# Optimization experiments

Hardware: AMD Instinct MI355X
Metric: run time of the kernel (lower is better)

## Reference

```python
import jax, jax.numpy as jnp
import numpy as np

B, C = 8388608, 4
OTHERS_IDX = 3

def setup_inputs() -> dict:
    key = jax.random.key(0)
    k1, k2 = jax.random.split(key)
    preds = jax.random.normal(k1, (B, C), dtype=jnp.float32)
    target = jax.random.randint(k2, (B,), 0, C, dtype=jnp.int64)
    return {"preds": preds, "target": target, "others_idx": OTHERS_IDX}

def reference(preds, target, others_idx):
    # softmax over class dim (dim=1 in the torch module)
    probs = jax.nn.softmax(preds, axis=1)              # [B, C]
    p_o = probs[:, others_idx]                          # [B]
    s = probs.sum(axis=1)                               # [B] (== 1, but computed as in original)
    # per-sample false-negative error (samples whose target IS the 'others' class)
    fne_i = 0.5 * ((s - p_o) ** 2 + (p_o - 1.0) ** 2)   # [B]
    # per-sample false-positive error (samples whose target is NOT 'others')
    fpe_i = 0.5 * ((-p_o) ** 2 + p_o ** 2)              # [B]
    is_others = (target == others_idx)                  # [B] bool
    fne_num = jnp.sum(is_others).astype(probs.dtype)
    fpe_num = jnp.sum(~is_others).astype(probs.dtype)
    fne = jnp.sum(jnp.where(is_others, fne_i, 0.0)) / fne_num
    fpe = jnp.sum(jnp.where(is_others, 0.0, fpe_i)) / fpe_num
    return fpe + fne
```

## Files before the change

kernel.cpp:

```cpp
#include <hip/hip_runtime.h>


#define BLOCK 1024
#define ROWS 16
#define CHUNK 4
#define STAGES (ROWS / CHUNK)

typedef float vfloat4 __attribute__((ext_vector_type(4)));

__device__ __forceinline__ void mfe_row(vfloat4 x, int t, int o,
                                        float& fne_acc, float& fpe_acc,
                                        float& cnt_acc) {
    float m = fmaxf(fmaxf(x.x, x.y), fmaxf(x.z, x.w));
    float e0 = __expf(x.x - m);
    float e1 = __expf(x.y - m);
    float e2 = __expf(x.z - m);
    float e3 = __expf(x.w - m);
    float S = (e0 + e1) + (e2 + e3);
    float r = 1.0f / S;
    float p0 = e0 * r, p1 = e1 * r, p2 = e2 * r, p3 = e3 * r;
    float s = ((p0 + p1) + p2) + p3;
    float po = (o == 0) ? p0 : (o == 1) ? p1 : (o == 2) ? p2 : p3;

    float d1 = s - po;
    float d2 = po - 1.0f;
    float fne_i = 0.5f * (d1 * d1 + d2 * d2);
    float fpe_i = po * po;

    bool is_o = (t == o);
    fne_acc += is_o ? fne_i : 0.0f;
    fpe_acc += is_o ? 0.0f : fpe_i;
    cnt_acc += is_o ? 1.0f : 0.0f;
}

__global__ __launch_bounds__(BLOCK) void mfe_partial(
    const vfloat4* __restrict__ preds,
    const int* __restrict__ target,
    const int* __restrict__ others_idx_p,
    float* __restrict__ fne_part,
    float* __restrict__ fpe_part,
    float* __restrict__ cnt_part,
    int n_rows)
{
    const int o = *others_idx_p;
    int tid = blockIdx.x * BLOCK + threadIdx.x;
    int nth = gridDim.x * BLOCK;

    float fne_acc = 0.0f, fpe_acc = 0.0f, cnt_acc = 0.0f;

    if (tid + (ROWS - 1) * nth < n_rows) {
        vfloat4 xbuf[2][CHUNK];
        int     tbuf[2][CHUNK];

        #pragma unroll
        for (int k = 0; k < CHUNK; ++k) {
            int i = tid + k * nth;
            xbuf[0][k] = __builtin_nontemporal_load(&preds[i]);
            tbuf[0][k] = __builtin_nontemporal_load(&target[i]);
        }

        #pragma unroll
        for (int s = 0; s < STAGES; ++s) {
            int cur = s & 1;
            int nxt = cur ^ 1;
            if (s + 1 < STAGES) {
                #pragma unroll
                for (int k = 0; k < CHUNK; ++k) {
                    int i = tid + ((s + 1) * CHUNK + k) * nth;
                    xbuf[nxt][k] = __builtin_nontemporal_load(&preds[i]);
                    tbuf[nxt][k] = __builtin_nontemporal_load(&target[i]);
                }
            }
            __builtin_amdgcn_sched_barrier(0);
            #pragma unroll
            for (int k = 0; k < CHUNK; ++k)
                mfe_row(xbuf[cur][k], tbuf[cur][k], o, fne_acc, fpe_acc, cnt_acc);
        }
    } else {
        for (int i = tid; i < n_rows; i += nth)
            mfe_row(preds[i], target[i], o, fne_acc, fpe_acc, cnt_acc);
    }

    #pragma unroll
    for (int off = 32; off > 0; off >>= 1) {
        fne_acc += __shfl_down(fne_acc, off, 64);
        fpe_acc += __shfl_down(fpe_acc, off, 64);
        cnt_acc += __shfl_down(cnt_acc, off, 64);
    }

    if ((threadIdx.x & 63) == 0) {
        int part = blockIdx.x * (BLOCK / 64) + (threadIdx.x >> 6);
        fne_part[part] = fne_acc;
        fpe_part[part] = fpe_acc;
        cnt_part[part] = cnt_acc;
    }
}

__global__ __launch_bounds__(1024) void mfe_final(
    const float* __restrict__ fne_part,
    const float* __restrict__ fpe_part,
    const float* __restrict__ cnt_part,
    int nparts, int n_rows, float* __restrict__ out)
{
    double fn = 0.0, fp = 0.0, c = 0.0;
    for (int i = threadIdx.x; i < nparts; i += blockDim.x) {
        fn += (double)fne_part[i];
        fp += (double)fpe_part[i];
        c  += (double)cnt_part[i];
    }
    #pragma unroll
    for (int off = 32; off > 0; off >>= 1) {
        fn += __shfl_down(fn, off, 64);
        fp += __shfl_down(fp, off, 64);
        c  += __shfl_down(c, off, 64);
    }
    __shared__ double s_fn[16], s_fp[16], s_c[16];
    int wave = threadIdx.x >> 6;
    int lane = threadIdx.x & 63;
    if (lane == 0) { s_fn[wave] = fn; s_fp[wave] = fp; s_c[wave] = c; }
    __syncthreads();

    if (threadIdx.x == 0) {
        double tfn = 0.0, tfp = 0.0, tc = 0.0;
        int nwaves = blockDim.x >> 6;
        for (int w = 0; w < nwaves; ++w) { tfn += s_fn[w]; tfp += s_fp[w]; tc += s_c[w]; }
        double fne_num = tc;
        double fpe_num = (double)n_rows - fne_num;
        double res = 0.0;
        if (fpe_num > 0.0) res += tfp / fpe_num;
        if (fne_num > 0.0) res += tfn / fne_num;
        out[0] = (float)res;
    }
}

extern "C" void kernel_launch(void* const* d_in, const int* in_sizes, int n_in,
                              void* d_out, int out_size, void* d_ws, size_t ws_size,
                              hipStream_t stream) {
    const vfloat4* preds = (const vfloat4*)d_in[0];
    const int* target = (const int*)d_in[1];
    const int* others_idx = (const int*)d_in[2];
    float* out = (float*)d_out;

    int n_rows = in_sizes[0] / 4;

    int grid = (n_rows + BLOCK * ROWS - 1) / (BLOCK * ROWS);
    int nparts = grid * (BLOCK / 64);

    float* fne_part = (float*)d_ws;
    float* fpe_part = fne_part + nparts;
    float* cnt_part = fpe_part + nparts;

    mfe_partial<<<grid, BLOCK, 0, stream>>>(preds, target, others_idx,
                                            fne_part, fpe_part, cnt_part, n_rows);
    mfe_final<<<1, 1024, 0, stream>>>(fne_part, fpe_part, cnt_part,
                                      nparts, n_rows, out);
}
```

Before: 202.9 us.

## Fuse final reduction into main kernel via last-block atomic ticket

Replaces the two-kernel reduction with a single kernel. Each block reduces its per-wave partials in shared memory, writes one double per quantity, and takes an atomic ticket. The last block to arrive performs the final reduction and writes the output. This removes the second kernel launch and its gap, but adds a memset launch for the ticket plus a fence and an atomic per block.

```diff
diff --git a/kernel.cpp b/kernel.cpp
--- a/kernel.cpp
+++ b/kernel.cpp
@@ -5,6 +5,7 @@
 #define ROWS 16
 #define CHUNK 4
 #define STAGES (ROWS / CHUNK)
+#define WAVES (BLOCK / 64)
 
 typedef float vfloat4 __attribute__((ext_vector_type(4)));
 
@@ -33,14 +34,16 @@
     cnt_acc += is_o ? 1.0f : 0.0f;
 }
 
-__global__ __launch_bounds__(BLOCK) void mfe_partial(
+__global__ __launch_bounds__(BLOCK) void mfe_fused(
     const vfloat4* __restrict__ preds,
     const int* __restrict__ target,
     const int* __restrict__ others_idx_p,
-    float* __restrict__ fne_part,
-    float* __restrict__ fpe_part,
-    float* __restrict__ cnt_part,
-    int n_rows)
+    double* __restrict__ fne_b,
+    double* __restrict__ fpe_b,
+    double* __restrict__ cnt_b,
+    unsigned* __restrict__ ticket,
+    int n_rows,
+    float* __restrict__ out)
 {
     const int o = *others_idx_p;
     int tid = blockIdx.x * BLOCK + threadIdx.x;
@@ -88,25 +91,37 @@
         cnt_acc += __shfl_down(cnt_acc, off, 64);
     }
 
-    if ((threadIdx.x & 63) == 0) {
-        int part = blockIdx.x * (BLOCK / 64) + (threadIdx.x >> 6);
-        fne_part[part] = fne_acc;
-        fpe_part[part] = fpe_acc;
-        cnt_part[part] = cnt_acc;
+    __shared__ double s_fn[WAVES], s_fp[WAVES], s_c[WAVES];
+    __shared__ int s_last;
+    int wave = threadIdx.x >> 6;
+    int lane = threadIdx.x & 63;
+    if (lane == 0) {
+        s_fn[wave] = (double)fne_acc;
+        s_fp[wave] = (double)fpe_acc;
+        s_c[wave]  = (double)cnt_acc;
     }
-}
+    __syncthreads();
 
-__global__ __launch_bounds__(1024) void mfe_final(
-    const float* __restrict__ fne_part,
-    const float* __restrict__ fpe_part,
-    const float* __restrict__ cnt_part,
-    int nparts, int n_rows, float* __restrict__ out)
-{
+    if (threadIdx.x == 0) {
+        double fn = 0.0, fp = 0.0, c = 0.0;
+        #pragma unroll
+        for (int w = 0; w < WAVES; ++w) { fn += s_fn[w]; fp += s_fp[w]; c += s_c[w]; }
+        fne_b[blockIdx.x] = fn;
+        fpe_b[blockIdx.x] = fp;
+        cnt_b[blockIdx.x] = c;
+        __threadfence();
+        unsigned t = __hip_atomic_fetch_add(ticket, 1u, __ATOMIC_ACQ_REL,
+                                            __HIP_MEMORY_SCOPE_AGENT);
+        s_last = (t == gridDim.x - 1) ? 1 : 0;
+    }
+    __syncthreads();
+    if (!s_last) return;
+
     double fn = 0.0, fp = 0.0, c = 0.0;
-    for (int i = threadIdx.x; i < nparts; i += blockDim.x) {
-        fn += (double)fne_part[i];
-        fp += (double)fpe_part[i];
-        c  += (double)cnt_part[i];
+    for (int i = threadIdx.x; i < (int)gridDim.x; i += BLOCK) {
+        fn += __hip_atomic_load(&fne_b[i], __ATOMIC_RELAXED, __HIP_MEMORY_SCOPE_AGENT);
+        fp += __hip_atomic_load(&fpe_b[i], __ATOMIC_RELAXED, __HIP_MEMORY_SCOPE_AGENT);
+        c  += __hip_atomic_load(&cnt_b[i], __ATOMIC_RELAXED, __HIP_MEMORY_SCOPE_AGENT);
     }
     #pragma unroll
     for (int off = 32; off > 0; off >>= 1) {
@@ -114,18 +129,16 @@
         fp += __shfl_down(fp, off, 64);
         c  += __shfl_down(c, off, 64);
     }
-    __shared__ double s_fn[16], s_fp[16], s_c[16];
-    int wave = threadIdx.x >> 6;
-    int lane = threadIdx.x & 63;
+    __syncthreads();
     if (lane == 0) { s_fn[wave] = fn; s_fp[wave] = fp; s_c[wave] = c; }
     __syncthreads();
 
     if (threadIdx.x == 0) {
         double tfn = 0.0, tfp = 0.0, tc = 0.0;
-        int nwaves = blockDim.x >> 6;
-        for (int w = 0; w < nwaves; ++w) { tfn += s_fn[w]; tfp += s_fp[w]; tc += s_c[w]; }
+        #pragma unroll
+        for (int w = 0; w < WAVES; ++w) { tfn += s_fn[w]; tfp += s_fp[w]; tc += s_c[w]; }
         double fne_num = tc;
-        double fpe_num = (double)n_rows - fne_num;
+        double fpe_num = (double)n_rows - tc;
         double res = 0.0;
         if (fpe_num > 0.0) res += tfp / fpe_num;
         if (fne_num > 0.0) res += tfn / fne_num;
@@ -144,14 +157,15 @@
     int n_rows = in_sizes[0] / 4;
 
     int grid = (n_rows + BLOCK * ROWS - 1) / (BLOCK * ROWS);
-    int nparts = grid * (BLOCK / 64);
 
-    float* fne_part = (float*)d_ws;
-    float* fpe_part = fne_part + nparts;
-    float* cnt_part = fpe_part + nparts;
+    double* fne_b = (double*)d_ws;
+    double* fpe_b = fne_b + grid;
+    double* cnt_b = fpe_b + grid;
+    unsigned* ticket = (unsigned*)(cnt_b + grid);
 
-    mfe_partial<<<grid, BLOCK, 0, stream>>>(preds, target, others_idx,
-                                            fne_part, fpe_part, cnt_part, n_rows);
-    mfe_final<<<1, 1024, 0, stream>>>(fne_part, fpe_part, cnt_part,
-                                      nparts, n_rows, out);
+    hipMemsetAsync(ticket, 0, sizeof(unsigned), stream);
+
+    mfe_fused<<<grid, BLOCK, 0, stream>>>(preds, target, others_idx,
+                                          fne_b, fpe_b, cnt_b, ticket,
+                                          n_rows, out);
 }
```

Result: slower. 220.0 us (+8.4%).
